# Kernel optimization log

Hardware: AMD Instinct MI355X
Metric: run time of the kernel (lower is better)

## Reference

```python
import jax, jax.numpy as jnp
import numpy as np

N, E = 50000, 800000          # nodes, edges
CUR, HID, OUT = 128, 128, 128  # cur_dim, hidden_dim, output_dim
NEG_SLOPE = 0.01               # F.leaky_relu default


def setup_inputs() -> dict:
    key = jax.random.key(0)
    ks = jax.random.split(key, 12)
    rn = lambda k, shp, s: jax.random.normal(k, shp, dtype=jnp.float32) * s
    s_c, s_h, s_o = 1.0 / np.sqrt(CUR), 1.0 / np.sqrt(HID), 1.0 / np.sqrt(OUT)
    return {
        "h": rn(ks[0], (N, CUR), 1.0),
        "x": rn(ks[1], (N, CUR), 1.0),
        "edge_index": jax.random.randint(ks[2], (2, E), 0, N, dtype=jnp.int32),
        "edge_weight": jax.random.uniform(ks[3], (E,), dtype=jnp.float32),
        # preprocessor_x: Linear(CUR, HID)
        "Wp": rn(ks[4], (HID, CUR), s_c), "bp": jnp.zeros((HID,), jnp.float32),
        # ChebConv(HID, OUT, K=2): two weight mats + bias
        "Wc0": rn(ks[5], (OUT, HID), s_h), "Wc1": rn(ks[6], (OUT, HID), s_h),
        "bc": jnp.zeros((OUT,), jnp.float32),
        # SAGEConv(HID, OUT): lin_rel (neighbors, with bias) + lin_root (self)
        "Wrel": rn(ks[7], (OUT, HID), s_h), "brel": jnp.zeros((OUT,), jnp.float32),
        "Wroot": rn(ks[8], (OUT, HID), s_h),
        # final Linear(OUT, OUT)
        "Wl": rn(ks[9], (OUT, OUT), s_o), "bl": jnp.zeros((OUT,), jnp.float32),
    }


def reference(h, x, edge_index, edge_weight, Wp, bp, Wc0, Wc1, bc,
              Wrel, brel, Wroot, Wl, bl):
    n = x.shape[0]
    src, dst = edge_index[0], edge_index[1]
    seg = lambda d, i: jax.ops.segment_sum(d, i, num_segments=n)

    his = x
    xh = x @ Wp.T + bp                               # [N, HID]

    # --- ChebConv, K=2, sym norm, lambda_max=2 => Lhat = -D^{-1/2} A D^{-1/2}
    deg = seg(edge_weight, src)                       # weighted degree
    dis = jnp.where(deg > 0, jax.lax.rsqrt(jnp.where(deg > 0, deg, 1.0)), 0.0)
    norm = -dis[src] * edge_weight * dis[dst]         # [E]
    Tx1 = seg(norm[:, None] * xh[src], dst)           # [N, HID]
    o1 = jax.nn.leaky_relu(xh @ Wc0.T + Tx1 @ Wc1.T + bc, NEG_SLOPE)

    # --- SAGEConv: mean of edge_weight-scaled neighbor feats + root transform
    msum = seg(edge_weight[:, None] * xh[src], dst)   # [N, HID]
    cnt = seg(jnp.ones_like(edge_weight), dst)        # in-degree
    mean = msum / jnp.maximum(cnt, 1.0)[:, None]
    o2 = jax.nn.leaky_relu(mean @ Wrel.T + brel + xh @ Wroot.T, NEG_SLOPE)

    o3 = (o1 + o2) @ Wl.T + bl
    return (his, o3)
```

## Files before the change

### kernel.cpp

```cpp
#include <hip/hip_runtime.h>

#define NN 50000
#define EE 800000
#define D  128
#define NCH 64
#define CH  12500
#define NR  8
#define RS  6250
#define KCA 64
#define KAB 576
#define XHB 782
#define CSB 196
#define PKB 384
#define FB  1563

typedef short short8 __attribute__((ext_vector_type(8)));
typedef float floatx4 __attribute__((ext_vector_type(4)));
typedef float floatx16 __attribute__((ext_vector_type(16)));

__device__ __forceinline__ float leaky(float v) { return v > 0.f ? v : 0.01f * v; }

__device__ __forceinline__ unsigned short f2bf(float f) {
    unsigned int u = __float_as_uint(f);
    u = (u + 0x7fff + ((u >> 16) & 1)) >> 16;
    return (unsigned short)u;
}
__device__ __forceinline__ float bf2f(unsigned int h) {
    return __uint_as_float(h << 16);
}

__global__ __launch_bounds__(256) void k_pre(
    const float* __restrict__ Wp,  const float* __restrict__ Wc0,
    const float* __restrict__ Wc1, const float* __restrict__ Wrel,
    const float* __restrict__ Wroot, const float* __restrict__ Wl,
    unsigned short* __restrict__ Pall) {
    int gid = blockIdx.x * 256 + threadIdx.x;
    int mm = gid >> 14;
    int r = gid & 16383;
    int j  = r & 7;
    int l  = (r >> 3) & 63;
    int n, k;
    if (mm == 0) {
        int ct = (r >> 9) & 7;
        int kc = r >> 12;
        n = ct * 16 + (l & 15);
        k = kc * 32 + (l >> 4) * 8 + j;
    } else {
        int ct = (r >> 9) & 3;
        int kc = (r >> 11) & 7;
        n = ct * 32 + (l & 31);
        k = kc * 16 + (l >> 5) * 8 + j;
    }
    const float* W = mm == 0 ? Wp : mm == 1 ? Wc0 : mm == 2 ? Wc1
                   : mm == 3 ? Wrel : mm == 4 ? Wroot : Wl;
    Pall[gid] = f2bf(W[n * 128 + k]);
}

__global__ __launch_bounds__(256) void k_main(
    const int* __restrict__ src, const int* __restrict__ dst,
    const float* __restrict__ ew,
    int* __restrict__ counts,
    float* __restrict__ degp,
    unsigned short* __restrict__ rank,
    const float* __restrict__ x, const float* __restrict__ bp,
    unsigned short* __restrict__ xh16, float* __restrict__ his,
    const unsigned short* __restrict__ Pall) {
    __shared__ __align__(16) unsigned int sbuf[12544];
    int b = blockIdx.x;
    if (b < KCA) {
        int c = b;
        for (int i = threadIdx.x; i < 12500; i += 256) sbuf[i] = 0u;
        __syncthreads();
        int base = c * CH;
        for (int i0 = threadIdx.x * 4; i0 < CH; i0 += 1024) {
            int e = base + i0;
            int4 d4 = *(const int4*)(dst + e);
            unsigned d, old;
            d = (unsigned)d4.x;
            old = atomicAdd(&sbuf[d >> 2], 1u << ((d & 3) * 8));
            rank[e]     = (unsigned short)((old >> ((d & 3) * 8)) & 0xffu);
            d = (unsigned)d4.y;
            old = atomicAdd(&sbuf[d >> 2], 1u << ((d & 3) * 8));
            rank[e + 1] = (unsigned short)((old >> ((d & 3) * 8)) & 0xffu);
            d = (unsigned)d4.z;
            old = atomicAdd(&sbuf[d >> 2], 1u << ((d & 3) * 8));
            rank[e + 2] = (unsigned short)((old >> ((d & 3) * 8)) & 0xffu);
            d = (unsigned)d4.w;
            old = atomicAdd(&sbuf[d >> 2], 1u << ((d & 3) * 8));
            rank[e + 3] = (unsigned short)((old >> ((d & 3) * 8)) & 0xffu);
        }
        __syncthreads();
        size_t ob = (size_t)c * NN;
        for (int i = threadIdx.x; i < NN; i += 256)
            counts[ob + i] = (int)((sbuf[i >> 2] >> ((i & 3) * 8)) & 0xffu);
    } else if (b < KAB) {
        int bb = b - KCA;
        int c = bb & 63;
        int rlo = (bb >> 6) * RS;
        float* sdeg = (float*)sbuf;
        for (int i = threadIdx.x; i < RS; i += 256) sdeg[i] = 0.f;
        __syncthreads();
        int base = c * CH;
        for (int i0 = threadIdx.x * 4; i0 < CH; i0 += 1024) {
            int e = base + i0;
            int4   s4 = *(const int4*)(src + e);
            float4 w4 = *(const float4*)(ew + e);
            unsigned sr;
            sr = (unsigned)(s4.x - rlo); if (sr < RS) atomicAdd(&sdeg[sr], w4.x);
            sr = (unsigned)(s4.y - rlo); if (sr < RS) atomicAdd(&sdeg[sr], w4.y);
            sr = (unsigned)(s4.z - rlo); if (sr < RS) atomicAdd(&sdeg[sr], w4.z);
            sr = (unsigned)(s4.w - rlo); if (sr < RS) atomicAdd(&sdeg[sr], w4.w);
        }
        __syncthreads();
        size_t ob = (size_t)c * NN + rlo;
        for (int i = threadIdx.x; i < RS; i += 256) degp[ob + i] = sdeg[i];
    } else {
        int bb = b - KAB;
        const unsigned short* Pp = Pall;
        int wave = threadIdx.x >> 6, l = threadIdx.x & 63;
        int n0 = bb * 64 + wave * 16;
        int m = l & 15, q = l >> 4;
        int nodeA = n0 + m;
        bool av = nodeA < NN;
        int na = av ? nodeA : 0;
        floatx4 acc[8];
#pragma unroll
        for (int ct = 0; ct < 8; ++ct) acc[ct] = (floatx4)(0.f);
#pragma unroll
        for (int kc = 0; kc < 4; ++kc) {
            const float* ap = x + (size_t)na * 128 + kc * 32 + q * 8;
            float4 f0 = av ? *(const float4*)ap       : make_float4(0, 0, 0, 0);
            float4 f1 = av ? *(const float4*)(ap + 4) : make_float4(0, 0, 0, 0);
            if (av) {
                float* hp = his + (size_t)nodeA * 128 + kc * 32 + q * 8;
                *(float4*)hp       = f0;
                *(float4*)(hp + 4) = f1;
            }
            short8 a;
            a[0] = f2bf(f0.x); a[1] = f2bf(f0.y); a[2] = f2bf(f0.z); a[3] = f2bf(f0.w);
            a[4] = f2bf(f1.x); a[5] = f2bf(f1.y); a[6] = f2bf(f1.z); a[7] = f2bf(f1.w);
#pragma unroll
            for (int ct = 0; ct < 8; ++ct) {
                short8 bfr = *(const short8*)(Pp + ((kc * 8 + ct) << 9) + l * 8);
                acc[ct] = __builtin_amdgcn_mfma_f32_16x16x32_bf16(a, bfr, acc[ct], 0, 0, 0);
            }
        }
#pragma unroll
        for (int ct = 0; ct < 8; ++ct) {
            int col = ct * 16 + m;
            float bias = bp[col];
#pragma unroll
            for (int r = 0; r < 4; ++r) {
                int node = n0 + q * 4 + r;
                if (node < NN) xh16[(size_t)node * 128 + col] = f2bf(acc[ct][r] + bias);
            }
        }
    }
}

__global__ __launch_bounds__(256) void k_colscan(int* __restrict__ counts,
                                                 const float* __restrict__ degp,
                                                 int* __restrict__ cntI,
                                                 float* __restrict__ deg,
                                                 int* __restrict__ blocksum) {
    __shared__ int ws4[4];
    int t = threadIdx.x;
    int n = blockIdx.x * 256 + t;
    int acc = 0; float dacc = 0.f;
    if (n < NN) {
#pragma unroll 8
        for (int c = 0; c < NCH; ++c) {
            size_t idx = (size_t)c * NN + n;
            int v = counts[idx];
            counts[idx] = acc;
            acc += v;
            dacc += degp[idx];
        }
        cntI[n] = acc;
        deg[n] = dacc;
    }
    int s = (n < NN) ? acc : 0;
#pragma unroll
    for (int off = 32; off > 0; off >>= 1) s += __shfl_down(s, off, 64);
    if ((t & 63) == 0) ws4[t >> 6] = s;
    __syncthreads();
    if (t == 0) blocksum[blockIdx.x] = ws4[0] + ws4[1] + ws4[2] + ws4[3];
}

__global__ __launch_bounds__(256) void k_scan_final(const int* __restrict__ cntI,
                                                    const int* __restrict__ blocksum,
                                                    int* __restrict__ rowstart) {
    __shared__ int sbs[256];
    __shared__ int wtot[4];
    int t = threadIdx.x, lane = t & 63, wave = t >> 6;
    int bv = (t < CSB) ? blocksum[t] : 0;
    int binc = bv;
#pragma unroll
    for (int off = 1; off < 64; off <<= 1) {
        int u = __shfl_up(binc, off, 64);
        if (lane >= off) binc += u;
    }
    if (lane == 63) wtot[wave] = binc;
    __syncthreads();
    int bpre = 0;
    for (int w = 0; w < wave; ++w) bpre += wtot[w];
    sbs[t] = binc + bpre;
    __syncthreads();
    int boff = (blockIdx.x == 0) ? 0 : sbs[blockIdx.x - 1];
    if (blockIdx.x == 0 && t == 0) rowstart[NN] = sbs[CSB - 1];
    int n = blockIdx.x * 256 + t;
    int v = (n < NN) ? cntI[n] : 0;
    int incl = v;
#pragma unroll
    for (int off = 1; off < 64; off <<= 1) {
        int u = __shfl_up(incl, off, 64);
        if (lane >= off) incl += u;
    }
    if (lane == 63) wtot[wave] = incl;
    __syncthreads();
    int wpre = 0;
    for (int w = 0; w < wave; ++w) wpre += wtot[w];
    incl += wpre;
    if (n < NN) rowstart[n] = boff + incl - v;
}

__global__ __launch_bounds__(256) void k_bucket(const int* __restrict__ src,
                                                const int* __restrict__ dst,
                                                const float* __restrict__ ew,
                                                const float* __restrict__ deg,
                                                const int* __restrict__ rowstart,
                                                const int* __restrict__ chunkoff,
                                                const unsigned short* __restrict__ rank,
                                                int4* __restrict__ rec) {
    int e = blockIdx.x * blockDim.x + threadIdx.x;
    if (e >= EE) return;
    int s = src[e], d = dst[e];
    float w = ew[e];
    float degs = deg[s];
    float dis_s = degs > 0.f ? rsqrtf(degs) : 0.f;
    int c = e / CH;
    int pos = rowstart[d] + chunkoff[(size_t)c * NN + d] + (int)rank[e];
    int4 r;
    r.x = s;
    r.y = __float_as_int(w);
    r.z = __float_as_int(dis_s * w);
    r.w = 0;
    rec[pos] = r;
}

__global__ __launch_bounds__(256) void k_gather(const int* __restrict__ rowstart,
                                                const int4* __restrict__ rec,
                                                const float* __restrict__ deg,
                                                const unsigned short* __restrict__ xh16,
                                                unsigned int* __restrict__ tx16,
                                                unsigned int* __restrict__ mn16) {
    int wave = threadIdx.x >> 6, l = threadIdx.x & 63;
    int n = blockIdx.x * 4 + wave;
    if (n >= NN) return;
    int lo = rowstart[n], hi = rowstart[n + 1];
    int half = l >> 5, c32 = l & 31;
    float am0 = 0.f, am1 = 0.f, am2 = 0.f, am3 = 0.f;
    float at0 = 0.f, at1 = 0.f, at2 = 0.f, at3 = 0.f;
    int e = lo + half;
    for (; e + 6 < hi; e += 8) {
        int4 r0 = rec[e], r1 = rec[e + 2], r2 = rec[e + 4], r3 = rec[e + 6];
        uint2 v0 = *(const uint2*)(xh16 + (size_t)r0.x * 128 + c32 * 4);
        uint2 v1 = *(const uint2*)(xh16 + (size_t)r1.x * 128 + c32 * 4);
        uint2 v2 = *(const uint2*)(xh16 + (size_t)r2.x * 128 + c32 * 4);
        uint2 v3 = *(const uint2*)(xh16 + (size_t)r3.x * 128 + c32 * 4);
        float w0 = __int_as_float(r0.y), u0 = __int_as_float(r0.z);
        float w1 = __int_as_float(r1.y), u1 = __int_as_float(r1.z);
        float w2 = __int_as_float(r2.y), u2 = __int_as_float(r2.z);
        float w3 = __int_as_float(r3.y), u3 = __int_as_float(r3.z);
        float a0, a1, a2, a3;
        a0 = bf2f(v0.x & 0xffff); a1 = bf2f(v0.x >> 16);
        a2 = bf2f(v0.y & 0xffff); a3 = bf2f(v0.y >> 16);
        am0 = fmaf(w0, a0, am0); am1 = fmaf(w0, a1, am1);
        am2 = fmaf(w0, a2, am2); am3 = fmaf(w0, a3, am3);
        at0 = fmaf(u0, a0, at0); at1 = fmaf(u0, a1, at1);
        at2 = fmaf(u0, a2, at2); at3 = fmaf(u0, a3, at3);
        a0 = bf2f(v1.x & 0xffff); a1 = bf2f(v1.x >> 16);
        a2 = bf2f(v1.y & 0xffff); a3 = bf2f(v1.y >> 16);
        am0 = fmaf(w1, a0, am0); am1 = fmaf(w1, a1, am1);
        am2 = fmaf(w1, a2, am2); am3 = fmaf(w1, a3, am3);
        at0 = fmaf(u1, a0, at0); at1 = fmaf(u1, a1, at1);
        at2 = fmaf(u1, a2, at2); at3 = fmaf(u1, a3, at3);
        a0 = bf2f(v2.x & 0xffff); a1 = bf2f(v2.x >> 16);
        a2 = bf2f(v2.y & 0xffff); a3 = bf2f(v2.y >> 16);
        am0 = fmaf(w2, a0, am0); am1 = fmaf(w2, a1, am1);
        am2 = fmaf(w2, a2, am2); am3 = fmaf(w2, a3, am3);
        at0 = fmaf(u2, a0, at0); at1 = fmaf(u2, a1, at1);
        at2 = fmaf(u2, a2, at2); at3 = fmaf(u2, a3, at3);
        a0 = bf2f(v3.x & 0xffff); a1 = bf2f(v3.x >> 16);
        a2 = bf2f(v3.y & 0xffff); a3 = bf2f(v3.y >> 16);
        am0 = fmaf(w3, a0, am0); am1 = fmaf(w3, a1, am1);
        am2 = fmaf(w3, a2, am2); am3 = fmaf(w3, a3, am3);
        at0 = fmaf(u3, a0, at0); at1 = fmaf(u3, a1, at1);
        at2 = fmaf(u3, a2, at2); at3 = fmaf(u3, a3, at3);
    }
    for (; e < hi; e += 2) {
        int4 r0 = rec[e];
        uint2 v0 = *(const uint2*)(xh16 + (size_t)r0.x * 128 + c32 * 4);
        float w0 = __int_as_float(r0.y), u0 = __int_as_float(r0.z);
        float a0 = bf2f(v0.x & 0xffff), a1 = bf2f(v0.x >> 16);
        float a2 = bf2f(v0.y & 0xffff), a3 = bf2f(v0.y >> 16);
        am0 = fmaf(w0, a0, am0); am1 = fmaf(w0, a1, am1);
        am2 = fmaf(w0, a2, am2); am3 = fmaf(w0, a3, am3);
        at0 = fmaf(u0, a0, at0); at1 = fmaf(u0, a1, at1);
        at2 = fmaf(u0, a2, at2); at3 = fmaf(u0, a3, at3);
    }
    am0 += __shfl_xor(am0, 32, 64); am1 += __shfl_xor(am1, 32, 64);
    am2 += __shfl_xor(am2, 32, 64); am3 += __shfl_xor(am3, 32, 64);
    at0 += __shfl_xor(at0, 32, 64); at1 += __shfl_xor(at1, 32, 64);
    at2 += __shfl_xor(at2, 32, 64); at3 += __shfl_xor(at3, 32, 64);
    float dd = deg[n];
    float dis_d = dd > 0.f ? rsqrtf(dd) : 0.f;
    int c = hi - lo;
    float ic = 1.f / (float)(c > 0 ? c : 1);
    if (half == 0) {
        uint2 t;
        t.x = (unsigned int)f2bf(-dis_d * at0) | ((unsigned int)f2bf(-dis_d * at1) << 16);
        t.y = (unsigned int)f2bf(-dis_d * at2) | ((unsigned int)f2bf(-dis_d * at3) << 16);
        *(uint2*)(tx16 + (size_t)n * 64 + c32 * 2) = t;
    } else {
        uint2 m;
        m.x = (unsigned int)f2bf(am0 * ic) | ((unsigned int)f2bf(am1 * ic) << 16);
        m.y = (unsigned int)f2bf(am2 * ic) | ((unsigned int)f2bf(am3 * ic) << 16);
        *(uint2*)(mn16 + (size_t)n * 64 + c32 * 2) = m;
    }
}

__global__ __launch_bounds__(256, 4) void k_fused(const unsigned short* __restrict__ xh16,
                                               const unsigned short* __restrict__ tx16,
                                               const unsigned short* __restrict__ mn16,
                                               const unsigned short* __restrict__ Pall,
                                               const float* __restrict__ bc,
                                               const float* __restrict__ brel,
                                               const float* __restrict__ bl,
                                               float* __restrict__ out) {
    const unsigned short* Pc0  = Pall + 1 * 16384;
    const unsigned short* Pc1  = Pall + 2 * 16384;
    const unsigned short* Prel = Pall + 3 * 16384;
    const unsigned short* Proot= Pall + 4 * 16384;
    const unsigned short* Pl   = Pall + 5 * 16384;
    __shared__ __align__(16) unsigned short sS[32][128];
    int ct = threadIdx.x >> 6, l = threadIdx.x & 63;
    int n0 = blockIdx.x * 32;
    int row = l & 31, half = l >> 5;
    int node = n0 + row;
    bool av = node < NN;
    size_t ra = (size_t)(av ? node : 0) * 128 + half * 8;
    floatx16 acc1 = (floatx16)(0.f), acc2 = (floatx16)(0.f);
#pragma unroll
    for (int kc = 0; kc < 8; ++kc) {
        short8 Axh = *(const short8*)(xh16 + ra + kc * 16);
        short8 Atx = *(const short8*)(tx16 + ra + kc * 16);
        short8 Amn = *(const short8*)(mn16 + ra + kc * 16);
        int po = ((kc * 4 + ct) << 9) + l * 8;
        short8 b0 = *(const short8*)(Pc0 + po);
        short8 b1 = *(const short8*)(Pc1 + po);
        short8 b2 = *(const short8*)(Prel + po);
        short8 b3 = *(const short8*)(Proot + po);
        acc1 = __builtin_amdgcn_mfma_f32_32x32x16_bf16(Axh, b0, acc1, 0, 0, 0);
        acc1 = __builtin_amdgcn_mfma_f32_32x32x16_bf16(Atx, b1, acc1, 0, 0, 0);
        acc2 = __builtin_amdgcn_mfma_f32_32x32x16_bf16(Amn, b2, acc2, 0, 0, 0);
        acc2 = __builtin_amdgcn_mfma_f32_32x32x16_bf16(Axh, b3, acc2, 0, 0, 0);
    }
    int col = ct * 32 + row;
    float b1v = bc[col], b2v = brel[col];
#pragma unroll
    for (int r = 0; r < 16; ++r) {
        int rr = (r & 3) + 8 * (r >> 2) + 4 * half;
        float u = leaky(acc1[r] + b1v) + leaky(acc2[r] + b2v);
        int sw = ((((col >> 3) ^ rr) & 15) << 3) | (col & 7);
        sS[rr][sw] = f2bf(u);
    }
    __syncthreads();
    floatx16 acc3 = (floatx16)(0.f);
#pragma unroll
    for (int kc = 0; kc < 8; ++kc) {
        int g = (kc * 2 + half) ^ (row & 15);
        short8 As = *(const short8*)&sS[row][g << 3];
        short8 b = *(const short8*)(Pl + ((kc * 4 + ct) << 9) + l * 8);
        acc3 = __builtin_amdgcn_mfma_f32_32x32x16_bf16(As, b, acc3, 0, 0, 0);
    }
    float bv = bl[col];
#pragma unroll
    for (int r = 0; r < 16; ++r) {
        int rr = (r & 3) + 8 * (r >> 2) + 4 * half;
        int nd = n0 + rr;
        if (nd < NN) out[(size_t)nd * 128 + col] = acc3[r] + bv;
    }
}

extern "C" void kernel_launch(void* const* d_in, const int* in_sizes, int n_in,
                              void* d_out, int out_size, void* d_ws, size_t ws_size,
                              hipStream_t stream) {
    const float* x    = (const float*)d_in[1];
    const int*   ei   = (const int*)d_in[2];
    const float* ew   = (const float*)d_in[3];
    const float* Wp   = (const float*)d_in[4];
    const float* bp   = (const float*)d_in[5];
    const float* Wc0  = (const float*)d_in[6];
    const float* Wc1  = (const float*)d_in[7];
    const float* bc   = (const float*)d_in[8];
    const float* Wrel = (const float*)d_in[9];
    const float* brel = (const float*)d_in[10];
    const float* Wroot= (const float*)d_in[11];
    const float* Wl   = (const float*)d_in[12];
    const float* bl   = (const float*)d_in[13];
    (void)in_sizes; (void)n_in; (void)out_size; (void)ws_size;
    float* out = (float*)d_out;

    unsigned short* xh16 = (unsigned short*)d_ws;
    unsigned short* tx16 = xh16 + (size_t)NN * 128;
    unsigned short* mn16 = tx16 + (size_t)NN * 128;
    unsigned short* Pall = mn16 + (size_t)NN * 128;
    int*   counts = (int*)(Pall + 6 * 16384);
    int4*  rec    = (int4*)(counts + (size_t)NCH * NN);
    float* degp   = (float*)rec;
    unsigned short* rank = (unsigned short*)(rec + EE);
    int*   rowstart = (int*)(rank + EE);
    int*   blocksum = rowstart + NN + 2;
    int*   blockoff = blocksum + CSB;
    int*   cntI   = blockoff + CSB;
    float* deg    = (float*)(cntI + NN);

    const int* srcI = ei;
    const int* dstI = ei + EE;

    k_pre<<<PKB, 256, 0, stream>>>(Wp, Wc0, Wc1, Wrel, Wroot, Wl, Pall);
    k_main<<<KAB + XHB, 256, 0, stream>>>(
        srcI, dstI, ew, counts, degp, rank, x, bp, xh16, out, Pall);
    k_colscan<<<CSB, 256, 0, stream>>>(counts, degp, cntI, deg, blocksum);
    k_scan_final<<<CSB, 256, 0, stream>>>(cntI, blocksum, rowstart);
    k_bucket<<<(EE + 255) / 256, 256, 0, stream>>>(srcI, dstI, ew, deg, rowstart,
                                                   counts, rank, rec);
    k_gather<<<(NN + 3) / 4, 256, 0, stream>>>(rowstart, rec, deg, xh16,
                                               (unsigned int*)tx16, (unsigned int*)mn16);
    k_fused<<<FB, 256, 0, stream>>>(xh16, tx16, mn16, Pall,
                                    bc, brel, bl, out + (size_t)NN * 128);
}
```

Baseline: 253.0 us.

## Fold weight packing into main kernel and unroll gather loop to 16 edges

Removes the separate weight-packing launch. The xh projection blocks now read and convert Wp to bf16 inline, and the other five weight matrices are packed by extra blocks appended to the main kernel's grid. This drops one kernel launch and its serialization, at the cost of redundant per-block conversion of Wp from fp32 global memory. The gather kernel also gets a 16-edge unrolled loop, which puts more independent loads in flight per iteration in exchange for higher register use.

```diff
diff --git a/kernel.cpp b/kernel.cpp
--- a/kernel.cpp
+++ b/kernel.cpp
@@ -9,9 +9,9 @@
 #define RS  6250
 #define KCA 64
 #define KAB 576
-#define XHB 782
+#define KABC 1358
+#define KALL 1678
 #define CSB 196
-#define PKB 384
 #define FB  1563
 
 typedef short short8 __attribute__((ext_vector_type(8)));
@@ -27,33 +27,6 @@
 }
 __device__ __forceinline__ float bf2f(unsigned int h) {
     return __uint_as_float(h << 16);
-}
-
-__global__ __launch_bounds__(256) void k_pre(
-    const float* __restrict__ Wp,  const float* __restrict__ Wc0,
-    const float* __restrict__ Wc1, const float* __restrict__ Wrel,
-    const float* __restrict__ Wroot, const float* __restrict__ Wl,
-    unsigned short* __restrict__ Pall) {
-    int gid = blockIdx.x * 256 + threadIdx.x;
-    int mm = gid >> 14;
-    int r = gid & 16383;
-    int j  = r & 7;
-    int l  = (r >> 3) & 63;
-    int n, k;
-    if (mm == 0) {
-        int ct = (r >> 9) & 7;
-        int kc = r >> 12;
-        n = ct * 16 + (l & 15);
-        k = kc * 32 + (l >> 4) * 8 + j;
-    } else {
-        int ct = (r >> 9) & 3;
-        int kc = (r >> 11) & 7;
-        n = ct * 32 + (l & 31);
-        k = kc * 16 + (l >> 5) * 8 + j;
-    }
-    const float* W = mm == 0 ? Wp : mm == 1 ? Wc0 : mm == 2 ? Wc1
-                   : mm == 3 ? Wrel : mm == 4 ? Wroot : Wl;
-    Pall[gid] = f2bf(W[n * 128 + k]);
 }
 
 __global__ __launch_bounds__(256) void k_main(
@@ -64,7 +37,10 @@
     unsigned short* __restrict__ rank,
     const float* __restrict__ x, const float* __restrict__ bp,
     unsigned short* __restrict__ xh16, float* __restrict__ his,
-    const unsigned short* __restrict__ Pall) {
+    const float* __restrict__ Wp,  const float* __restrict__ Wc0,
+    const float* __restrict__ Wc1, const float* __restrict__ Wrel,
+    const float* __restrict__ Wroot, const float* __restrict__ Wl,
+    unsigned short* __restrict__ Pall) {
     __shared__ __align__(16) unsigned int sbuf[12544];
     int b = blockIdx.x;
     if (b < KCA) {
@@ -114,9 +90,8 @@
         __syncthreads();
         size_t ob = (size_t)c * NN + rlo;
         for (int i = threadIdx.x; i < RS; i += 256) degp[ob + i] = sdeg[i];
-    } else {
+    } else if (b < KABC) {
         int bb = b - KAB;
-        const unsigned short* Pp = Pall;
         int wave = threadIdx.x >> 6, l = threadIdx.x & 63;
         int n0 = bb * 64 + wave * 16;
         int m = l & 15, q = l >> 4;
@@ -141,7 +116,12 @@
             a[4] = f2bf(f1.x); a[5] = f2bf(f1.y); a[6] = f2bf(f1.z); a[7] = f2bf(f1.w);
 #pragma unroll
             for (int ct = 0; ct < 8; ++ct) {
-                short8 bfr = *(const short8*)(Pp + ((kc * 8 + ct) << 9) + l * 8);
+                const float* wp = Wp + (ct * 16 + m) * 128 + kc * 32 + q * 8;
+                float4 w0 = *(const float4*)wp;
+                float4 w1 = *(const float4*)(wp + 4);
+                short8 bfr;
+                bfr[0] = f2bf(w0.x); bfr[1] = f2bf(w0.y); bfr[2] = f2bf(w0.z); bfr[3] = f2bf(w0.w);
+                bfr[4] = f2bf(w1.x); bfr[5] = f2bf(w1.y); bfr[6] = f2bf(w1.z); bfr[7] = f2bf(w1.w);
                 acc[ct] = __builtin_amdgcn_mfma_f32_16x16x32_bf16(a, bfr, acc[ct], 0, 0, 0);
             }
         }
@@ -155,6 +135,19 @@
                 if (node < NN) xh16[(size_t)node * 128 + col] = f2bf(acc[ct][r] + bias);
             }
         }
+    } else {
+        int pgid = (b - KABC) * 256 + threadIdx.x;
+        int mm = 1 + (pgid >> 14);
+        int r = pgid & 16383;
+        int j  = r & 7;
+        int l  = (r >> 3) & 63;
+        int ct = (r >> 9) & 3;
+        int kc = (r >> 11) & 7;
+        int n = ct * 32 + (l & 31);
+        int k = kc * 16 + (l >> 5) * 8 + j;
+        const float* W = mm == 1 ? Wc0 : mm == 2 ? Wc1
+                       : mm == 3 ? Wrel : mm == 4 ? Wroot : Wl;
+        Pall[(size_t)mm * 16384 + r] = f2bf(W[n * 128 + k]);
     }
 }
 
@@ -262,53 +255,45 @@
     float am0 = 0.f, am1 = 0.f, am2 = 0.f, am3 = 0.f;
     float at0 = 0.f, at1 = 0.f, at2 = 0.f, at3 = 0.f;
     int e = lo + half;
+    for (; e + 14 < hi; e += 16) {
+        int4 r0 = rec[e],      r1 = rec[e + 2],  r2 = rec[e + 4],  r3 = rec[e + 6];
+        int4 r4 = rec[e + 8],  r5 = rec[e + 10], r6 = rec[e + 12], r7 = rec[e + 14];
+        uint2 v0 = *(const uint2*)(xh16 + (size_t)r0.x * 128 + c32 * 4);
+        uint2 v1 = *(const uint2*)(xh16 + (size_t)r1.x * 128 + c32 * 4);
+        uint2 v2 = *(const uint2*)(xh16 + (size_t)r2.x * 128 + c32 * 4);
+        uint2 v3 = *(const uint2*)(xh16 + (size_t)r3.x * 128 + c32 * 4);
+        uint2 v4 = *(const uint2*)(xh16 + (size_t)r4.x * 128 + c32 * 4);
+        uint2 v5 = *(const uint2*)(xh16 + (size_t)r5.x * 128 + c32 * 4);
+        uint2 v6 = *(const uint2*)(xh16 + (size_t)r6.x * 128 + c32 * 4);
+        uint2 v7 = *(const uint2*)(xh16 + (size_t)r7.x * 128 + c32 * 4);
+        float a0, a1, a2, a3, w0, u0;
+#define GACC(rr, vv)                                                           \
+        w0 = __int_as_float(rr.y); u0 = __int_as_float(rr.z);                  \
+        a0 = bf2f(vv.x & 0xffff); a1 = bf2f(vv.x >> 16);                       \
+        a2 = bf2f(vv.y & 0xffff); a3 = bf2f(vv.y >> 16);                       \
+        am0 = fmaf(w0, a0, am0); am1 = fmaf(w0, a1, am1);                      \
+        am2 = fmaf(w0, a2, am2); am3 = fmaf(w0, a3, am3);                      \
+        at0 = fmaf(u0, a0, at0); at1 = fmaf(u0, a1, at1);                      \
+        at2 = fmaf(u0, a2, at2); at3 = fmaf(u0, a3, at3);
+        GACC(r0, v0) GACC(r1, v1) GACC(r2, v2) GACC(r3, v3)
+        GACC(r4, v4) GACC(r5, v5) GACC(r6, v6) GACC(r7, v7)
+    }
     for (; e + 6 < hi; e += 8) {
         int4 r0 = rec[e], r1 = rec[e + 2], r2 = rec[e + 4], r3 = rec[e + 6];
         uint2 v0 = *(const uint2*)(xh16 + (size_t)r0.x * 128 + c32 * 4);
         uint2 v1 = *(const uint2*)(xh16 + (size_t)r1.x * 128 + c32 * 4);
         uint2 v2 = *(const uint2*)(xh16 + (size_t)r2.x * 128 + c32 * 4);
         uint2 v3 = *(const uint2*)(xh16 + (size_t)r3.x * 128 + c32 * 4);
-        float w0 = __int_as_float(r0.y), u0 = __int_as_float(r0.z);
-        float w1 = __int_as_float(r1.y), u1 = __int_as_float(r1.z);
-        float w2 = __int_as_float(r2.y), u2 = __int_as_float(r2.z);
-        float w3 = __int_as_float(r3.y), u3 = __int_as_float(r3.z);
-        float a0, a1, a2, a3;
-        a0 = bf2f(v0.x & 0xffff); a1 = bf2f(v0.x >> 16);
-        a2 = bf2f(v0.y & 0xffff); a3 = bf2f(v0.y >> 16);
-        am0 = fmaf(w0, a0, am0); am1 = fmaf(w0, a1, am1);
-        am2 = fmaf(w0, a2, am2); am3 = fmaf(w0, a3, am3);
-        at0 = fmaf(u0, a0, at0); at1 = fmaf(u0, a1, at1);
-        at2 = fmaf(u0, a2, at2); at3 = fmaf(u0, a3, at3);
-        a0 = bf2f(v1.x & 0xffff); a1 = bf2f(v1.x >> 16);
-        a2 = bf2f(v1.y & 0xffff); a3 = bf2f(v1.y >> 16);
-        am0 = fmaf(w1, a0, am0); am1 = fmaf(w1, a1, am1);
-        am2 = fmaf(w1, a2, am2); am3 = fmaf(w1, a3, am3);
-        at0 = fmaf(u1, a0, at0); at1 = fmaf(u1, a1, at1);
-        at2 = fmaf(u1, a2, at2); at3 = fmaf(u1, a3, at3);
-        a0 = bf2f(v2.x & 0xffff); a1 = bf2f(v2.x >> 16);
-        a2 = bf2f(v2.y & 0xffff); a3 = bf2f(v2.y >> 16);
-        am0 = fmaf(w2, a0, am0); am1 = fmaf(w2, a1, am1);
-        am2 = fmaf(w2, a2, am2); am3 = fmaf(w2, a3, am3);
-        at0 = fmaf(u2, a0, at0); at1 = fmaf(u2, a1, at1);
-        at2 = fmaf(u2, a2, at2); at3 = fmaf(u2, a3, at3);
-        a0 = bf2f(v3.x & 0xffff); a1 = bf2f(v3.x >> 16);
-        a2 = bf2f(v3.y & 0xffff); a3 = bf2f(v3.y >> 16);
-        am0 = fmaf(w3, a0, am0); am1 = fmaf(w3, a1, am1);
-        am2 = fmaf(w3, a2, am2); am3 = fmaf(w3, a3, am3);
-        at0 = fmaf(u3, a0, at0); at1 = fmaf(u3, a1, at1);
-        at2 = fmaf(u3, a2, at2); at3 = fmaf(u3, a3, at3);
+        float a0, a1, a2, a3, w0, u0;
+        GACC(r0, v0) GACC(r1, v1) GACC(r2, v2) GACC(r3, v3)
     }
     for (; e < hi; e += 2) {
         int4 r0 = rec[e];
         uint2 v0 = *(const uint2*)(xh16 + (size_t)r0.x * 128 + c32 * 4);
-        float w0 = __int_as_float(r0.y), u0 = __int_as_float(r0.z);
-        float a0 = bf2f(v0.x & 0xffff), a1 = bf2f(v0.x >> 16);
-        float a2 = bf2f(v0.y & 0xffff), a3 = bf2f(v0.y >> 16);
-        am0 = fmaf(w0, a0, am0); am1 = fmaf(w0, a1, am1);
-        am2 = fmaf(w0, a2, am2); am3 = fmaf(w0, a3, am3);
-        at0 = fmaf(u0, a0, at0); at1 = fmaf(u0, a1, at1);
-        at2 = fmaf(u0, a2, at2); at3 = fmaf(u0, a3, at3);
-    }
+        float a0, a1, a2, a3, w0, u0;
+        GACC(r0, v0)
+    }
+#undef GACC
     am0 += __shfl_xor(am0, 32, 64); am1 += __shfl_xor(am1, 32, 64);
     am2 += __shfl_xor(am2, 32, 64); am3 += __shfl_xor(am3, 32, 64);
     at0 += __shfl_xor(at0, 32, 64); at1 += __shfl_xor(at1, 32, 64);
@@ -429,9 +414,9 @@
     const int* srcI = ei;
     const int* dstI = ei + EE;
 
-    k_pre<<<PKB, 256, 0, stream>>>(Wp, Wc0, Wc1, Wrel, Wroot, Wl, Pall);
-    k_main<<<KAB + XHB, 256, 0, stream>>>(
-        srcI, dstI, ew, counts, degp, rank, x, bp, xh16, out, Pall);
+    k_main<<<KALL, 256, 0, stream>>>(
+        srcI, dstI, ew, counts, degp, rank, x, bp, xh16, out,
+        Wp, Wc0, Wc1, Wrel, Wroot, Wl, Pall);
     k_colscan<<<CSB, 256, 0, stream>>>(counts, degp, cntI, deg, blocksum);
     k_scan_final<<<CSB, 256, 0, stream>>>(cntI, blocksum, rowstart);
     k_bucket<<<(EE + 255) / 256, 256, 0, stream>>>(srcI, dstI, ew, deg, rowstart,
```

After: 271.0 us. 1.07x slower.
